# Performance work log

Hardware: AMD Instinct MI355X
Metric: run time of the kernel (lower is better)

## Reference

```python
import jax, jax.numpy as jnp
import numpy as np
from jax import lax

H, W, C = 24, 8, 128
HW = H * W
PART = 4
SA_K = 49  # CBAM spatial-attention kernel size (default of CBAMBlock)
EPS = 1e-5


def conv2d(x, w, b, pad_h, pad_w):
    y = lax.conv_general_dilated(x, w, (1, 1), [(pad_h, pad_h), (pad_w, pad_w)],
                                 dimension_numbers=('NCHW', 'OIHW', 'NCHW'))
    return y + b[None, :, None, None]


def cbam(x, se_w1, se_w2, sa_w, sa_b):
    # Channel attention: shared MLP on global max- and avg-pooled descriptors.
    mx = x.max(axis=(2, 3))          # [n, c]
    av = x.mean(axis=(2, 3))         # [n, c]
    def se(v):
        return jax.nn.relu(v @ se_w1.T) @ se_w2.T
    ca = jax.nn.sigmoid(se(mx) + se(av))[:, :, None, None]
    out = x * ca
    # Spatial attention: 49x49 conv on [max, mean] over channels.
    smx = out.max(axis=1, keepdims=True)
    sav = out.mean(axis=1, keepdims=True)
    s = jnp.concatenate([smx, sav], axis=1)      # [n, 2, H, W]
    sa = jax.nn.sigmoid(conv2d(s, sa_w, sa_b, SA_K // 2, SA_K // 2))
    return out * sa + x


def position_aware_max(score6, dim):
    # score6: [p, g, hr, wr, hs, ws]; fixed-length (part_rows) row window,
    # start clamped to [0, h - part_rows] -> vectorized sliding-window max.
    part_rows = H // PART
    half = part_rows // 2
    starts = jnp.clip(jnp.arange(H) - half, 0, H - part_rows)
    if dim == 0:
        m = score6.max(axis=3)            # max over wr -> [p, g, hr, hs, ws]
        mi = jnp.moveaxis(m, 3, 0)        # [hs, p, g, hr, ws]
        def f(m_i, st):
            return lax.dynamic_slice_in_dim(m_i, st, part_rows, axis=2).max(axis=2)
        out = jax.vmap(f)(mi, starts)     # [h, p, g, ws]
    else:
        m = score6.max(axis=5)            # max over ws -> [p, g, hr, wr, hs]
        mi = jnp.moveaxis(m, 2, 0)        # [hr, p, g, wr, hs]
        def f(m_i, st):
            return lax.dynamic_slice_in_dim(m_i, st, part_rows, axis=3).max(axis=3)
        out = jax.vmap(f)(mi, starts)     # [h, p, g, wr]
    p, g = score6.shape[0], score6.shape[1]
    return jnp.moveaxis(out, 0, 2).reshape(p, g, HW)


def bn_eval(x, gamma, beta, mean, var):
    return (x - mean) * (gamma / jnp.sqrt(var + EPS)) + beta


def setup_inputs() -> dict:
    key = jax.random.key(0)
    ks = jax.random.split(key, 8)
    red = 16
    return {
        'prob_fea': jax.random.normal(ks[0], (32, C, H, W), jnp.float32),
        'gal_fea': jax.random.normal(ks[1], (32, C, H, W), jnp.float32),
        'se_w1': jax.random.normal(ks[2], (C // red, C), jnp.float32) * 0.05,
        'se_w2': jax.random.normal(ks[3], (C, C // red), jnp.float32) * 0.05,
        'sa_w': jax.random.normal(ks[4], (1, 2, SA_K, SA_K), jnp.float32) * 0.02,
        'sa_b': jnp.zeros((1,), jnp.float32),
        'bn_g': jnp.ones((1,), jnp.float32),
        'bn_b': jnp.zeros((1,), jnp.float32),
        'bn_m': jnp.zeros((1,), jnp.float32),
        'bn_v': jnp.ones((1,), jnp.float32),
        'fc_w': jnp.full((1, HW), 1.0 / HW, jnp.float32),
        'fc_b': jax.random.normal(ks[5], (1,), jnp.float32) * 0.01,
        'lbn_g': jnp.ones((1,), jnp.float32),
        'lbn_b': jnp.zeros((1,), jnp.float32),
        'lbn_m': jnp.zeros((1,), jnp.float32),
        'lbn_v': jnp.ones((1,), jnp.float32),
    }


def reference(prob_fea, gal_fea, se_w1, se_w2, sa_w, sa_b,
              bn_g, bn_b, bn_m, bn_v, fc_w, fc_b,
              lbn_g, lbn_b, lbn_m, lbn_v):
    pf = cbam(prob_fea, se_w1, se_w2, sa_w, sa_b)
    gf = cbam(gal_fea, se_w1, se_w2, sa_w, sa_b)
    p, g = pf.shape[0], gf.shape[0]
    pf = pf.reshape(p, C, HW)
    gf = gf.reshape(g, C, HW)
    # pairwise feature matching: [p, g, r(gal spatial), s(prob spatial)]
    score = jnp.einsum('pcs,gcr->pgrs', pf, gf)
    score6 = score.reshape(p, g, H, W, H, W)
    s1 = position_aware_max(score6, 0)  # [p, g, HW]
    s2 = position_aware_max(score6, 1)  # [p, g, HW]
    sc = jnp.concatenate([s1, s2], axis=-1).reshape(-1, HW)  # [p*g*2, HW]
    sc = bn_eval(sc, bn_g, bn_b, bn_m, bn_v)
    y = sc @ fc_w.T + fc_b                  # [p*g*2, 1]
    y = y.reshape(-1, 2).sum(axis=1, keepdims=True)
    y = bn_eval(y, lbn_g, lbn_b, lbn_m, lbn_v)
    return jax.nn.sigmoid(y).reshape(p, g)
```

## Files before the change

### kernel.cpp

```cpp
#include <hip/hip_runtime.h>
#include <hip/hip_bf16.h>

#define HH 24
#define WW 8
#define HWSZ 192
#define CC 128
#define EPSV 1e-5f

#define M1LD 200
#define M2LD 28

typedef __attribute__((ext_vector_type(8))) short bf16x8;
typedef __attribute__((ext_vector_type(4))) float f32x4;

__device__ __forceinline__ float sigmoidf_(float x) { return 1.0f / (1.0f + expf(-x)); }

__device__ __forceinline__ unsigned short f2bf(float f) {
    unsigned int u = __float_as_uint(f);
    unsigned int r = (u + 0x7fffu + ((u >> 16) & 1u)) >> 16;
    return (unsigned short)r;
}
__device__ __forceinline__ float bf2f(unsigned short s) {
    return __uint_as_float((unsigned int)s << 16);
}

__global__ __launch_bounds__(512) void cbam_kernel(
    const float* __restrict__ prob, const float* __restrict__ gal,
    const float* __restrict__ se_w1, const float* __restrict__ se_w2,
    const float* __restrict__ sa_w, const float* __restrict__ sa_b,
    __hip_bfloat16* __restrict__ pf_t, __hip_bfloat16* __restrict__ gf_t)
{
    __shared__ float mxs[CC], avs[CC], hid[16], cas[CC];
    __shared__ float smx2[2 * HWSZ], sav2[2 * HWSZ], sas[HWSZ];
    __shared__ float wbuf[2 * 49 * 49];

    int n = blockIdx.x;
    const float* x = (n < 32) ? prob + (size_t)n * CC * HWSZ : gal + (size_t)(n - 32) * CC * HWSZ;
    __hip_bfloat16* dst = (n < 32) ? pf_t + (size_t)n * HWSZ * CC : gf_t + (size_t)(n - 32) * HWSZ * CC;

    int tid = threadIdx.x, l = tid & 63, w = tid >> 6;

    for (int i = tid; i < 2 * 49 * 49; i += 512) wbuf[i] = sa_w[i];

    for (int i = 0; i < 16; ++i) {
        int c = w * 16 + i;
        const float* row = x + c * HWSZ;
        float a = row[l], b = row[l + 64], d = row[l + 128];
        float mv = fmaxf(a, fmaxf(b, d));
        float sv = a + b + d;
        #pragma unroll
        for (int m = 1; m < 64; m <<= 1) {
            mv = fmaxf(mv, __shfl_xor(mv, m));
            sv += __shfl_xor(sv, m);
        }
        if (l == 0) { mxs[c] = mv; avs[c] = sv * (1.0f / HWSZ); }
    }
    __syncthreads();

    if (tid < 256) {
        int j = tid >> 4, chunk = tid & 15;
        const float* v = (j < 8) ? mxs : avs;
        const float* wrow = se_w1 + (j & 7) * CC + chunk * 8;
        const float* vv = v + chunk * 8;
        float acc = 0.f;
        #pragma unroll
        for (int k = 0; k < 8; ++k) acc += vv[k] * wrow[k];
        #pragma unroll
        for (int m = 1; m < 16; m <<= 1) acc += __shfl_xor(acc, m);
        if (chunk == 0) hid[j] = fmaxf(acc, 0.f);
    }
    __syncthreads();

    if (tid < CC) {
        float acc = 0.f;
        #pragma unroll
        for (int j = 0; j < 8; ++j) acc += (hid[j] + hid[8 + j]) * se_w2[tid * 8 + j];
        cas[tid] = sigmoidf_(acc);
    }
    __syncthreads();

    if (tid < 2 * HWSZ) {
        int s = tid >> 1, half = tid & 1;
        int c0 = half * 64;
        float mv = -INFINITY, sv = 0.f;
        #pragma unroll 4
        for (int k = 0; k < 64; ++k) {
            float v = x[(c0 + k) * HWSZ + s] * cas[c0 + k];
            mv = fmaxf(mv, v); sv += v;
        }
        smx2[half * HWSZ + s] = mv; sav2[half * HWSZ + s] = sv;
    }
    __syncthreads();

    if (tid < HWSZ) {
        int y = tid >> 3, xx = tid & 7;
        float acc = sa_b[0];
        for (int iy = 0; iy < HH; ++iy) {
            int wy = iy - y + 24;
            const float* w0 = wbuf + wy * 49;
            const float* w1 = wbuf + 2401 + wy * 49;
            #pragma unroll
            for (int ix = 0; ix < WW; ++ix) {
                int wx = ix - xx + 24;
                int sp = iy * 8 + ix;
                float s0 = fmaxf(smx2[sp], smx2[HWSZ + sp]);
                float s1 = (sav2[sp] + sav2[HWSZ + sp]) * (1.0f / CC);
                acc += s0 * w0[wx] + s1 * w1[wx];
            }
        }
        sas[tid] = sigmoidf_(acc);
    }
    __syncthreads();

    if (tid < 2 * HWSZ) {
        int s = tid >> 1, half = tid & 1;
        int c0 = half * 64;
        float sv = sas[s];
        unsigned int* dst32 = (unsigned int*)(dst + s * CC) + half * 32;
        #pragma unroll 4
        for (int k = 0; k < 32; ++k) {
            int c = c0 + 2 * k;
            float v0 = x[c * HWSZ + s] * (1.f + cas[c] * sv);
            float v1 = x[(c + 1) * HWSZ + s] * (1.f + cas[c + 1] * sv);
            dst32[k] = ((unsigned int)f2bf(v1) << 16) | (unsigned int)f2bf(v0);
        }
    }
}

__global__ __launch_bounds__(384) void score_kernel(
    const __hip_bfloat16* __restrict__ pf_t, const __hip_bfloat16* __restrict__ gf_t,
    const float* __restrict__ bn_g, const float* __restrict__ bn_b,
    const float* __restrict__ bn_m, const float* __restrict__ bn_v,
    const float* __restrict__ fc_w, const float* __restrict__ fc_b,
    const float* __restrict__ lbn_g, const float* __restrict__ lbn_b,
    const float* __restrict__ lbn_m, const float* __restrict__ lbn_v,
    float* __restrict__ out)
{
    __shared__ unsigned short M1b[24 * M1LD];
    __shared__ unsigned short M2b[HWSZ * M2LD];
    __shared__ float red[6], wred[6];

    int bi = blockIdx.x;
    int p = bi >> 5, g = bi & 31;
    int tid = threadIdx.x, l = tid & 63, w = tid >> 6;

    const __hip_bfloat16* A = gf_t + (size_t)g * HWSZ * CC;
    const __hip_bfloat16* B = pf_t + (size_t)p * HWSZ * CC;

    int row_a = l & 15;
    int koff = (l >> 4) * 8;

    bf16x8 afr[2][4];
    #pragma unroll
    for (int rt = 0; rt < 2; ++rt) {
        const __hip_bfloat16* ap = A + (w * 32 + rt * 16 + row_a) * CC + koff;
        #pragma unroll
        for (int ks = 0; ks < 4; ++ks)
            afr[rt][ks] = *(const bf16x8*)(ap + ks * 32);
    }

    bf16x8 b0, b1, b2, b3;
    {
        const __hip_bfloat16* bp = B + row_a * CC + koff;
        b0 = *(const bf16x8*)(bp);
        b1 = *(const bf16x8*)(bp + 32);
        b2 = *(const bf16x8*)(bp + 64);
        b3 = *(const bf16x8*)(bp + 96);
    }

    for (int st = 0; st < 12; ++st) {
        bf16x8 n0, n1, n2, n3;
        if (st < 11) {
            const __hip_bfloat16* bp = B + ((st + 1) * 16 + row_a) * CC + koff;
            n0 = *(const bf16x8*)(bp);
            n1 = *(const bf16x8*)(bp + 32);
            n2 = *(const bf16x8*)(bp + 64);
            n3 = *(const bf16x8*)(bp + 96);
        }

        #pragma unroll
        for (int rt = 0; rt < 2; ++rt) {
            f32x4 acc = {0.f, 0.f, 0.f, 0.f};
            acc = __builtin_amdgcn_mfma_f32_16x16x32_bf16(afr[rt][0], b0, acc, 0, 0, 0);
            acc = __builtin_amdgcn_mfma_f32_16x16x32_bf16(afr[rt][1], b1, acc, 0, 0, 0);
            acc = __builtin_amdgcn_mfma_f32_16x16x32_bf16(afr[rt][2], b2, acc, 0, 0, 0);
            acc = __builtin_amdgcn_mfma_f32_16x16x32_bf16(afr[rt][3], b3, acc, 0, 0, 0);

            int RT = w * 2 + rt;

            float mrow = fmaxf(fmaxf(acc[0], acc[1]), fmaxf(acc[2], acc[3]));
            mrow = fmaxf(mrow, __shfl_xor(mrow, 16));
            if (((l >> 4) & 1) == 0)
                M1b[(2 * RT + (l >> 5)) * M1LD + st * 16 + (l & 15)] = f2bf(mrow);

            float v0 = acc[0], v1 = acc[1], v2 = acc[2], v3 = acc[3];
            #pragma unroll
            for (int m = 1; m < 8; m <<= 1) {
                v0 = fmaxf(v0, __shfl_xor(v0, m));
                v1 = fmaxf(v1, __shfl_xor(v1, m));
                v2 = fmaxf(v2, __shfl_xor(v2, m));
                v3 = fmaxf(v3, __shfl_xor(v3, m));
            }
            if ((l & 7) == 0) {
                int hs = st * 2 + ((l >> 3) & 1);
                int rbase = RT * 16 + (l >> 4) * 4;
                M2b[(rbase + 0) * M2LD + hs] = f2bf(v0);
                M2b[(rbase + 1) * M2LD + hs] = f2bf(v1);
                M2b[(rbase + 2) * M2LD + hs] = f2bf(v2);
                M2b[(rbase + 3) * M2LD + hs] = f2bf(v3);
            }
        }
        b0 = n0; b1 = n1; b2 = n2; b3 = n3;
    }
    __syncthreads();

    float part = 0.f, wpart = 0.f;
    if (tid < HWSZ) {
        int h = tid >> 3;
        int st0 = h - 3; if (st0 < 0) st0 = 0; if (st0 > 18) st0 = 18;
        float v1 = -INFINITY, v2 = -INFINITY;
        #pragma unroll
        for (int i = 0; i < 6; ++i) {
            v1 = fmaxf(v1, bf2f(M1b[(st0 + i) * M1LD + tid]));
            v2 = fmaxf(v2, bf2f(M2b[tid * M2LD + st0 + i]));
        }
        float fw = fc_w[tid];
        part = fw * (v1 + v2);
        wpart = fw;
    }
    #pragma unroll
    for (int m = 1; m < 64; m <<= 1) {
        part  += __shfl_xor(part, m);
        wpart += __shfl_xor(wpart, m);
    }
    if (l == 0) { red[w] = part; wred[w] = wpart; }
    __syncthreads();

    if (tid == 0) {
        float total = red[0] + red[1] + red[2] + red[3] + red[4] + red[5];
        float Wsum  = wred[0] + wred[1] + wred[2] + wred[3] + wred[4] + wred[5];
        float k1 = bn_g[0] * rsqrtf(bn_v[0] + EPSV);
        float Y = k1 * total + 2.f * ((bn_b[0] - k1 * bn_m[0]) * Wsum + fc_b[0]);
        float kl = lbn_g[0] * rsqrtf(lbn_v[0] + EPSV);
        float Z = (Y - lbn_m[0]) * kl + lbn_b[0];
        out[bi] = 1.f / (1.f + expf(-Z));
    }
}

extern "C" void kernel_launch(void* const* d_in, const int* in_sizes, int n_in,
                              void* d_out, int out_size, void* d_ws, size_t ws_size,
                              hipStream_t stream)
{
    const float* prob  = (const float*)d_in[0];
    const float* gal   = (const float*)d_in[1];
    const float* se_w1 = (const float*)d_in[2];
    const float* se_w2 = (const float*)d_in[3];
    const float* sa_w  = (const float*)d_in[4];
    const float* sa_b  = (const float*)d_in[5];
    const float* bn_g  = (const float*)d_in[6];
    const float* bn_b  = (const float*)d_in[7];
    const float* bn_m  = (const float*)d_in[8];
    const float* bn_v  = (const float*)d_in[9];
    const float* fc_w  = (const float*)d_in[10];
    const float* fc_b  = (const float*)d_in[11];
    const float* lbn_g = (const float*)d_in[12];
    const float* lbn_b = (const float*)d_in[13];
    const float* lbn_m = (const float*)d_in[14];
    const float* lbn_v = (const float*)d_in[15];

    __hip_bfloat16* pf_t = (__hip_bfloat16*)d_ws;
    __hip_bfloat16* gf_t = pf_t + (size_t)32 * HWSZ * CC;
    float* out = (float*)d_out;

    cbam_kernel<<<64, 512, 0, stream>>>(prob, gal, se_w1, se_w2, sa_w, sa_b, pf_t, gf_t);
    score_kernel<<<1024, 384, 0, stream>>>(pf_t, gf_t, bn_g, bn_b, bn_m, bn_v,
                                           fc_w, fc_b, lbn_g, lbn_b, lbn_m, lbn_v, out);
}
```

Measured before the change: 153.6 us.

## Split CBAM into stats and apply kernels; stage B tiles via LDS

Moves the final CBAM scaling and bf16 transpose into a separate 768-block kernel that uses vectorized float4 loads and an LDS transpose, so the write-out of 64 images is no longer done by only 64 blocks. Channel and spatial attention values are passed between kernels through workspace buffers. In the score kernel, the per-wave B fragment loads are replaced with double-buffered global_load_lds staging shared across waves, with a block barrier on every step. The trade-offs are an extra kernel launch and extra synchronisation in the inner loop.

Result: no change. 154.0 us (+0.3%).

```diff
diff --git a/kernel.cpp b/kernel.cpp
--- a/kernel.cpp
+++ b/kernel.cpp
@@ -24,19 +24,18 @@
     return __uint_as_float((unsigned int)s << 16);
 }
 
-__global__ __launch_bounds__(512) void cbam_kernel(
+__global__ __launch_bounds__(512) void cbam_stats(
     const float* __restrict__ prob, const float* __restrict__ gal,
     const float* __restrict__ se_w1, const float* __restrict__ se_w2,
     const float* __restrict__ sa_w, const float* __restrict__ sa_b,
-    __hip_bfloat16* __restrict__ pf_t, __hip_bfloat16* __restrict__ gf_t)
+    float* __restrict__ ca_out, float* __restrict__ sa_out)
 {
     __shared__ float mxs[CC], avs[CC], hid[16], cas[CC];
-    __shared__ float smx2[2 * HWSZ], sav2[2 * HWSZ], sas[HWSZ];
+    __shared__ float smx2[2 * HWSZ], sav2[2 * HWSZ];
     __shared__ float wbuf[2 * 49 * 49];
 
     int n = blockIdx.x;
     const float* x = (n < 32) ? prob + (size_t)n * CC * HWSZ : gal + (size_t)(n - 32) * CC * HWSZ;
-    __hip_bfloat16* dst = (n < 32) ? pf_t + (size_t)n * HWSZ * CC : gf_t + (size_t)(n - 32) * HWSZ * CC;
 
     int tid = threadIdx.x, l = tid & 63, w = tid >> 6;
 
@@ -76,6 +75,7 @@
         #pragma unroll
         for (int j = 0; j < 8; ++j) acc += (hid[j] + hid[8 + j]) * se_w2[tid * 8 + j];
         cas[tid] = sigmoidf_(acc);
+        ca_out[n * CC + tid] = cas[tid];
     }
     __syncthreads();
 
@@ -108,23 +108,47 @@
                 acc += s0 * w0[wx] + s1 * w1[wx];
             }
         }
-        sas[tid] = sigmoidf_(acc);
-    }
-    __syncthreads();
-
-    if (tid < 2 * HWSZ) {
-        int s = tid >> 1, half = tid & 1;
-        int c0 = half * 64;
-        float sv = sas[s];
-        unsigned int* dst32 = (unsigned int*)(dst + s * CC) + half * 32;
-        #pragma unroll 4
-        for (int k = 0; k < 32; ++k) {
-            int c = c0 + 2 * k;
-            float v0 = x[c * HWSZ + s] * (1.f + cas[c] * sv);
-            float v1 = x[(c + 1) * HWSZ + s] * (1.f + cas[c + 1] * sv);
-            dst32[k] = ((unsigned int)f2bf(v1) << 16) | (unsigned int)f2bf(v0);
-        }
-    }
+        sa_out[n * HWSZ + tid] = sigmoidf_(acc);
+    }
+}
+
+__global__ __launch_bounds__(256) void cbam_apply(
+    const float* __restrict__ prob, const float* __restrict__ gal,
+    const float* __restrict__ ca_buf, const float* __restrict__ sa_buf,
+    __hip_bfloat16* __restrict__ pf_t, __hip_bfloat16* __restrict__ gf_t)
+{
+    __shared__ unsigned short T[16][136];
+    __shared__ float sash[16];
+
+    int n = blockIdx.x / 12;
+    int s0 = (blockIdx.x % 12) * 16;
+    const float* x = (n < 32) ? prob + (size_t)n * CC * HWSZ : gal + (size_t)(n - 32) * CC * HWSZ;
+    __hip_bfloat16* dst = (n < 32) ? pf_t + (size_t)n * HWSZ * CC : gf_t + (size_t)(n - 32) * HWSZ * CC;
+
+    int tid = threadIdx.x;
+    if (tid < 16) sash[tid] = sa_buf[n * HWSZ + s0 + tid];
+    __syncthreads();
+
+    int c = tid >> 1, half = tid & 1;
+    float ca = ca_buf[n * CC + c];
+    const float* xp = x + c * HWSZ + s0 + half * 8;
+    float4 va = *(const float4*)xp;
+    float4 vb = *(const float4*)(xp + 4);
+    int r0 = half * 8;
+    T[r0 + 0][c] = f2bf(va.x * (1.f + ca * sash[r0 + 0]));
+    T[r0 + 1][c] = f2bf(va.y * (1.f + ca * sash[r0 + 1]));
+    T[r0 + 2][c] = f2bf(va.z * (1.f + ca * sash[r0 + 2]));
+    T[r0 + 3][c] = f2bf(va.w * (1.f + ca * sash[r0 + 3]));
+    T[r0 + 4][c] = f2bf(vb.x * (1.f + ca * sash[r0 + 4]));
+    T[r0 + 5][c] = f2bf(vb.y * (1.f + ca * sash[r0 + 5]));
+    T[r0 + 6][c] = f2bf(vb.z * (1.f + ca * sash[r0 + 6]));
+    T[r0 + 7][c] = f2bf(vb.w * (1.f + ca * sash[r0 + 7]));
+    __syncthreads();
+
+    int s_l = tid >> 4, c8 = (tid & 15) * 8;
+    const unsigned int* src = (const unsigned int*)&T[s_l][c8];
+    unsigned int* d32 = (unsigned int*)(dst + (s0 + s_l) * CC + c8);
+    d32[0] = src[0]; d32[1] = src[1]; d32[2] = src[2]; d32[3] = src[3];
 }
 
 __global__ __launch_bounds__(384) void score_kernel(
@@ -136,6 +160,7 @@
     const float* __restrict__ lbn_m, const float* __restrict__ lbn_v,
     float* __restrict__ out)
 {
+    __shared__ __align__(16) char bstage[2][4096];
     __shared__ unsigned short M1b[24 * M1LD];
     __shared__ unsigned short M2b[HWSZ * M2LD];
     __shared__ float red[6], wred[6];
@@ -149,6 +174,18 @@
 
     int row_a = l & 15;
     int koff = (l >> 4) * 8;
+
+    #define STAGE_B(bufidx, st_)                                                         \
+        if (w < 4) {                                                                     \
+            const __hip_bfloat16* src = B + ((st_) * 16 + (l & 15)) * CC                 \
+                                          + (w * 4 + (l >> 4)) * 8;                      \
+            __builtin_amdgcn_global_load_lds(                                            \
+                (const __attribute__((address_space(1))) void*)src,                      \
+                (__attribute__((address_space(3))) void*)(&bstage[bufidx][w * 1024]),    \
+                16, 0, 0);                                                               \
+        }
+
+    STAGE_B(0, 0)
 
     bf16x8 afr[2][4];
     #pragma unroll
@@ -158,25 +195,17 @@
         for (int ks = 0; ks < 4; ++ks)
             afr[rt][ks] = *(const bf16x8*)(ap + ks * 32);
     }
-
-    bf16x8 b0, b1, b2, b3;
-    {
-        const __hip_bfloat16* bp = B + row_a * CC + koff;
-        b0 = *(const bf16x8*)(bp);
-        b1 = *(const bf16x8*)(bp + 32);
-        b2 = *(const bf16x8*)(bp + 64);
-        b3 = *(const bf16x8*)(bp + 96);
-    }
+    __syncthreads();
 
     for (int st = 0; st < 12; ++st) {
-        bf16x8 n0, n1, n2, n3;
-        if (st < 11) {
-            const __hip_bfloat16* bp = B + ((st + 1) * 16 + row_a) * CC + koff;
-            n0 = *(const bf16x8*)(bp);
-            n1 = *(const bf16x8*)(bp + 32);
-            n2 = *(const bf16x8*)(bp + 64);
-            n3 = *(const bf16x8*)(bp + 96);
-        }
+        int cur = st & 1;
+        if (st < 11) { STAGE_B(cur ^ 1, st + 1) }
+
+        const char* bb = bstage[cur];
+        bf16x8 b0 = *(const bf16x8*)(bb + 0 * 1024 + l * 16);
+        bf16x8 b1 = *(const bf16x8*)(bb + 1 * 1024 + l * 16);
+        bf16x8 b2 = *(const bf16x8*)(bb + 2 * 1024 + l * 16);
+        bf16x8 b3 = *(const bf16x8*)(bb + 3 * 1024 + l * 16);
 
         #pragma unroll
         for (int rt = 0; rt < 2; ++rt) {
@@ -210,9 +239,8 @@
                 M2b[(rbase + 3) * M2LD + hs] = f2bf(v3);
             }
         }
-        b0 = n0; b1 = n1; b2 = n2; b3 = n3;
-    }
-    __syncthreads();
+        __syncthreads();
+    }
 
     float part = 0.f, wpart = 0.f;
     if (tid < HWSZ) {
@@ -270,9 +298,12 @@
 
     __hip_bfloat16* pf_t = (__hip_bfloat16*)d_ws;
     __hip_bfloat16* gf_t = pf_t + (size_t)32 * HWSZ * CC;
+    float* ca_buf = (float*)(gf_t + (size_t)32 * HWSZ * CC);
+    float* sa_buf = ca_buf + 64 * CC;
     float* out = (float*)d_out;
 
-    cbam_kernel<<<64, 512, 0, stream>>>(prob, gal, se_w1, se_w2, sa_w, sa_b, pf_t, gf_t);
+    cbam_stats<<<64, 512, 0, stream>>>(prob, gal, se_w1, se_w2, sa_w, sa_b, ca_buf, sa_buf);
+    cbam_apply<<<768, 256, 0, stream>>>(prob, gal, ca_buf, sa_buf, pf_t, gf_t);
     score_kernel<<<1024, 384, 0, stream>>>(pf_t, gf_t, bn_g, bn_b, bn_m, bn_v,
                                            fc_w, fc_b, lbn_g, lbn_b, lbn_m, lbn_v, out);
 }
```
